# Kernel tuning notes

Measured on AMD Instinct MI355X. Metric: run time of the kernel, lower is better.

Reference implementation:

```python
import jax, jax.numpy as jnp
import numpy as np

HEADS = 16
EPS = 1e-5  # nn.LayerNorm default


def setup_inputs() -> dict:
    key = jax.random.key(0)
    ks = jax.random.split(key, 3)
    b, n, dim = 4, 1024, 1024
    x = jax.random.normal(ks[0], (b, n, dim), jnp.float32)
    ln_gamma = jnp.ones((dim,), jnp.float32)
    ln_beta = jnp.zeros((dim,), jnp.float32)
    # torch.nn.Linear stores weight as [out_features, in_features]
    w_qkv = jax.random.normal(ks[1], (3 * dim, dim), jnp.float32) * (dim ** -0.5)
    w_out = jax.random.normal(ks[2], (dim, dim), jnp.float32) * (dim ** -0.5)
    b_out = jnp.zeros((dim,), jnp.float32)
    return {"x": x, "ln_gamma": ln_gamma, "ln_beta": ln_beta,
            "w_qkv": w_qkv, "w_out": w_out, "b_out": b_out, "topk": 32}


def reference(x, ln_gamma, ln_beta, w_qkv, w_out, b_out, topk):
    b, n, dim = x.shape
    h = HEADS
    d = dim // h
    scale = d ** -0.5  # (inner_dim/heads)^-0.5 with inner_dim=dim

    # LayerNorm (biased variance, matching torch)
    mu = x.mean(-1, keepdims=True)
    var = x.var(-1, keepdims=True)
    xn = (x - mu) * jax.lax.rsqrt(var + EPS) * ln_gamma + ln_beta

    # qkv projection (no bias): y = x @ W^T
    qkv = jnp.einsum('bnd,ed->bne', xn, w_qkv)  # [b, n, 3*dim]
    q, k, v = jnp.split(qkv, 3, axis=-1)
    split_heads = lambda t: t.reshape(b, n, h, d).transpose(0, 2, 1, 3)  # [b,h,n,d]
    q = split_heads(q) * scale
    k = split_heads(k)
    v = split_heads(v)

    sim = jnp.einsum('bhid,bhjd->bhij', q, k)          # [b,h,n,n]
    attn = jax.nn.softmax(sim, axis=-1)
    # top-k SELECTION: probability values are discarded, only indices used
    _, idx = jax.lax.top_k(attn, topk)                 # [b,h,n,topk]
    # gather v rows at top-k indices and sum (unweighted), matching
    # torch.gather(vv, 2, idx).sum(-2)
    gathered = jnp.take_along_axis(
        v, idx.reshape(b, h, n * topk)[..., None], axis=2)  # [b,h,n*topk,d]
    xsum = gathered.reshape(b, h, n, topk, d).sum(axis=3)   # [b,h,n,d]

    # global min/max normalization then exp
    xmin = xsum.min()
    xmax = xsum.max()
    out = jnp.exp((xsum - xmin) / (xmax - xmin))

    out = out.transpose(0, 2, 1, 3).reshape(b, n, dim)  # b h n d -> b n (h d)
    # final projection (self.out Linear; Dropout(0.2) inert at eval)
    return jnp.einsum('bnd,ed->bne', out, w_out) + b_out
```

## Files before the change

### kernel.cpp

```cpp
#include <hip/hip_runtime.h>


#define LN_EPS 1e-5f

using half8   = __attribute__((ext_vector_type(8))) _Float16;
using half4   = __attribute__((ext_vector_type(4))) _Float16;
using float4v = __attribute__((ext_vector_type(4))) float;

__device__ __forceinline__ void gload_lds16(const void* g, void* l) {
  __builtin_amdgcn_global_load_lds(
      (const __attribute__((address_space(1))) void*)g,
      (__attribute__((address_space(3))) void*)l, 16, 0, 0);
}
__device__ __forceinline__ float4v mfma16(half8 a, half8 b, float4v c) {
  return __builtin_amdgcn_mfma_f32_16x16x32_f16(a, b, c, 0, 0, 0);
}
struct HL { _Float16 h, l; };
__device__ __forceinline__ HL split2(float x) {
  _Float16 h = (_Float16)x;
  return { h, (_Float16)(x - (float)h) };
}
__device__ __forceinline__ int mbcnt(unsigned long long m) {
  return __builtin_amdgcn_mbcnt_hi((unsigned)(m >> 32),
         __builtin_amdgcn_mbcnt_lo((unsigned)m, 0u));
}

__device__ __forceinline__ unsigned fkey(float f) {
  unsigned u = __float_as_uint(f);
  return ((int)u < 0) ? ~u : (u | 0x80000000u);
}
__device__ __forceinline__ int enc_i(float f) {
  int i = __float_as_int(f);
  return i >= 0 ? i : (i ^ 0x7fffffff);
}
__device__ __forceinline__ float dec_i(int e) {
  return __int_as_float(e >= 0 ? e : (e ^ 0x7fffffff));
}

__global__ __launch_bounds__(256)
void prep_kernel(const float* __restrict__ x, const float* __restrict__ gamma,
                 const float* __restrict__ beta,
                 _Float16* __restrict__ xh, _Float16* __restrict__ xl,
                 const float* __restrict__ wqkv, const float* __restrict__ wout,
                 _Float16* __restrict__ wqh, _Float16* __restrict__ wql,
                 _Float16* __restrict__ woh, _Float16* __restrict__ wol,
                 int* __restrict__ minmax) {
  int blk = blockIdx.x, t = threadIdx.x;
  if (blk < 4096) {
    __shared__ float red[8];
    int row = blk;
    const float4* xr = (const float4*)(x + (size_t)row * 1024);
    float4 v = xr[t];
    float s  = v.x + v.y + v.z + v.w;
    float s2 = v.x*v.x + v.y*v.y + v.z*v.z + v.w*v.w;
    #pragma unroll
    for (int o = 32; o >= 1; o >>= 1) {
      s  += __shfl_xor(s,  o, 64);
      s2 += __shfl_xor(s2, o, 64);
    }
    int w = t >> 6, l = t & 63;
    if (l == 0) { red[w*2] = s; red[w*2+1] = s2; }
    __syncthreads();
    float S  = red[0] + red[2] + red[4] + red[6];
    float S2 = red[1] + red[3] + red[5] + red[7];
    float mu  = S * (1.0f/1024.0f);
    float var = S2 * (1.0f/1024.0f) - mu*mu;
    float r = rsqrtf(var + LN_EPS);
    float4 g  = ((const float4*)gamma)[t];
    float4 bb = ((const float4*)beta)[t];
    float o0 = (v.x - mu) * r * g.x + bb.x;
    float o1 = (v.y - mu) * r * g.y + bb.y;
    float o2 = (v.z - mu) * r * g.z + bb.z;
    float o3 = (v.w - mu) * r * g.w + bb.w;
    HL r0 = split2(o0), r1 = split2(o1), r2 = split2(o2), r3 = split2(o3);
    half4 hh = { r0.h, r1.h, r2.h, r3.h };
    half4 ll = { r0.l, r1.l, r2.l, r3.l };
    size_t e = (size_t)row * 1024 + t*4;
    *(half4*)(xh + e) = hh;
    *(half4*)(xl + e) = ll;
  } else if (blk < 8192) {
    size_t i4 = (size_t)(blk - 4096) * 256 + t;
    const float* src; _Float16 *dh, *dl; size_t off;
    if (i4 < 786432) { src = wqkv; dh = wqh; dl = wql; off = i4; }
    else             { src = wout; dh = woh; dl = wol; off = i4 - 786432; }
    float4 v = ((const float4*)src)[off];
    HL r0 = split2(v.x), r1 = split2(v.y), r2 = split2(v.z), r3 = split2(v.w);
    half4 hh = { r0.h, r1.h, r2.h, r3.h };
    half4 ll = { r0.l, r1.l, r2.l, r3.l };
    ((half4*)dh)[off] = hh;
    ((half4*)dl)[off] = ll;
  } else if (t == 0) {
    minmax[0] = 0x7fffffff;
    minmax[1] = (int)0x80000000;
  }
}

template<int MODE, int NT>
__global__ __launch_bounds__(256)
void gemm_f16split(const _Float16* __restrict__ Ah, const _Float16* __restrict__ Al,
                   const _Float16* __restrict__ Bh, const _Float16* __restrict__ Bl,
                   const float* __restrict__ bias, float* __restrict__ CO,
                   _Float16* __restrict__ QH, _Float16* __restrict__ QL,
                   _Float16* __restrict__ KH, _Float16* __restrict__ KL,
                   float* __restrict__ CV) {
  constexpr int NV = NT / 32;
  __shared__ __align__(16) _Float16 lds[8192 + 2 * NT * 32];
  const int K = 1024;
  int tid = threadIdx.x, w = tid >> 6, l = tid & 63;
  int m0 = blockIdx.y * 128, n0 = blockIdx.x * NT;
  int wm = (w >> 1) * 64, wn = (w & 1) * (NT / 2);

  const _Float16* src = (w == 0) ? Ah : (w == 1) ? Al : (w == 2) ? Bh : Bl;
  int rowbase = (w < 2) ? m0 : n0;
  int iters   = (w < 2) ? 8 : NT / 16;
  _Float16* dst = lds + ((w < 2) ? (size_t)w * 4096
                                 : (size_t)8192 + (size_t)(w - 2) * NT * 32);
  int sr = l >> 2, sc = l & 3;

  float4v acc[4][NV];
  #pragma unroll
  for (int u = 0; u < 4; ++u)
    #pragma unroll
    for (int vv = 0; vv < NV; ++vv) acc[u][vv] = (float4v){0.f, 0.f, 0.f, 0.f};

  int quad = l >> 4, lo16 = l & 15;
  for (int kt = 0; kt < K; kt += 32) {
    __syncthreads();
    for (int i = 0; i < iters; ++i) {
      int row = i * 16 + sr;
      gload_lds16(src + (size_t)(rowbase + row) * K + kt + sc * 8,
                  dst + row * 32 + sc * 8);
    }
    __syncthreads();
    half8 ah[4], al[4], bh[NV], bl[NV];
    #pragma unroll
    for (int u = 0; u < 4; ++u) {
      int mrow = wm + u * 16 + lo16;
      ah[u] = *(const half8*)&lds[        (size_t)mrow * 32 + quad * 8];
      al[u] = *(const half8*)&lds[ 4096 + (size_t)mrow * 32 + quad * 8];
    }
    #pragma unroll
    for (int vv = 0; vv < NV; ++vv) {
      int nrow = wn + vv * 16 + lo16;
      bh[vv] = *(const half8*)&lds[8192           + (size_t)nrow * 32 + quad * 8];
      bl[vv] = *(const half8*)&lds[8192 + NT * 32 + (size_t)nrow * 32 + quad * 8];
    }
    #pragma unroll
    for (int u = 0; u < 4; ++u)
      #pragma unroll
      for (int vv = 0; vv < NV; ++vv) {
        acc[u][vv] = mfma16(ah[u], bh[vv], acc[u][vv]);
        acc[u][vv] = mfma16(ah[u], bl[vv], acc[u][vv]);
        acc[u][vv] = mfma16(al[u], bh[vv], acc[u][vv]);
      }
  }

  #pragma unroll
  for (int u = 0; u < 4; ++u) {
    #pragma unroll
    for (int vv = 0; vv < NV; ++vv) {
      #pragma unroll
      for (int rg = 0; rg < 4; ++rg) {
        int row = m0 + wm + u * 16 + quad * 4 + rg;
        int col = n0 + wn + vv * 16 + lo16;
        float val = acc[u][vv][rg];
        if (MODE == 0) {
          int which = col >> 10, h = (col >> 6) & 15, dd = col & 63;
          int b = row >> 10, i = row & 1023;
          size_t e = ((size_t)(b * 16 + h) << 16) + ((size_t)i << 6) + dd;
          if (which == 2) { CV[e] = val; }
          else {
            HL sp = split2(val);
            if (which == 0) { QH[e] = sp.h; QL[e] = sp.l; }
            else            { KH[e] = sp.h; KL[e] = sp.l; }
          }
        } else {
          CO[(size_t)row * 1024 + col] = val + bias[col];
        }
      }
    }
  }
}

__global__ __launch_bounds__(1024)
void attn_kernel(const _Float16* __restrict__ qh, const _Float16* __restrict__ ql,
                 const _Float16* __restrict__ kh, const _Float16* __restrict__ kl,
                 const float* __restrict__ vg, float* __restrict__ xsum) {
  __shared__ float simb[16][1028];
  __shared__ int sel[16][32];
  int g = blockIdx.x;
  int xcd = g & 7, slot = g >> 3;
  int bh = (slot >> 6) * 8 + xcd, grp = slot & 63;
  int tid = threadIdx.x, w = tid >> 6, l = tid & 63;
  int quad = l >> 4, lo16 = l & 15;
  size_t hb = (size_t)bh << 16;

  const _Float16* qhp = qh + hb + ((size_t)(grp * 16 + lo16) << 6);
  const _Float16* qlp = ql + hb + ((size_t)(grp * 16 + lo16) << 6);
  half8 ah0 = *(const half8*)(qhp + quad * 8);
  half8 ah1 = *(const half8*)(qhp + 32 + quad * 8);
  half8 al0 = *(const half8*)(qlp + quad * 8);
  half8 al1 = *(const half8*)(qlp + 32 + quad * 8);

  const _Float16* khp = kh + hb;
  const _Float16* klp = kl + hb;
  int jbase = w * 64;

  #pragma unroll
  for (int tt = 0; tt < 4; ++tt) {
    size_t off = ((size_t)(jbase + tt * 16 + lo16) << 6) + quad * 8;
    half8 b0 = *(const half8*)(khp + off);
    half8 b1 = *(const half8*)(khp + off + 32);
    half8 c0 = *(const half8*)(klp + off);
    half8 c1 = *(const half8*)(klp + off + 32);
    float4v acc = (float4v){0.f, 0.f, 0.f, 0.f};
    acc = mfma16(ah0, b0, acc);
    acc = mfma16(ah0, c0, acc);
    acc = mfma16(al0, b0, acc);
    acc = mfma16(ah1, b1, acc);
    acc = mfma16(ah1, c1, acc);
    acc = mfma16(al1, b1, acc);
    int jc = jbase + tt * 16 + lo16;
    #pragma unroll
    for (int rg = 0; rg < 4; ++rg)
      simb[quad * 4 + rg][jc] = acc[rg];
  }
  __syncthreads();

  unsigned ku[16];
  #pragma unroll
  for (int s = 0; s < 16; ++s) ku[s] = fkey(simb[w][s * 64 + l]);

  unsigned cur = 0u;
  bool exact = false;
  for (int bit = 31; bit >= 0; --bit) {
    unsigned T = cur | (1u << bit);
    int c = 0;
    #pragma unroll
    for (int s = 0; s < 16; ++s) c += __popcll(__ballot(ku[s] >= T));
    if (c >= 32) {
      cur = T;
      if (c == 32) { exact = true; break; }
    }
  }

  int base = 0;
  if (exact) {
    #pragma unroll
    for (int s = 0; s < 16; ++s) {
      bool take = ku[s] >= cur;
      unsigned long long mtk = __ballot(take);
      if (take) sel[w][base + mbcnt(mtk)] = s * 64 + l;
      base += __popcll(mtk);
    }
  } else {
    int gcnt = 0;
    #pragma unroll
    for (int s = 0; s < 16; ++s) gcnt += __popcll(__ballot(ku[s] > cur));
    int need = 32 - gcnt;
    int eqb = 0;
    #pragma unroll
    for (int s = 0; s < 16; ++s) {
      bool gt = ku[s] > cur;
      bool eq = ku[s] == cur;
      unsigned long long meq = __ballot(eq);
      int eqr = eqb + mbcnt(meq);
      bool take = gt || (eq && (eqr < need));
      unsigned long long mtk = __ballot(take);
      if (take) sel[w][base + mbcnt(mtk)] = s * 64 + l;
      base += __popcll(mtk);
      eqb  += __popcll(meq);
    }
  }

  const float* vb = vg + hb;
  int lg = l >> 4, lc = (l & 15) * 4;
  float4 vacc = {0.f, 0.f, 0.f, 0.f};
  #pragma unroll
  for (int p = 0; p < 8; ++p) {
    int j = sel[w][p * 4 + lg];
    float4 t = *(const float4*)(vb + ((size_t)j << 6) + lc);
    vacc.x += t.x; vacc.y += t.y; vacc.z += t.z; vacc.w += t.w;
  }
  #pragma unroll
  for (int o = 32; o >= 16; o >>= 1) {
    vacc.x += __shfl_xor(vacc.x, o, 64);
    vacc.y += __shfl_xor(vacc.y, o, 64);
    vacc.z += __shfl_xor(vacc.z, o, 64);
    vacc.w += __shfl_xor(vacc.w, o, 64);
  }
  if (l < 16)
    *(float4*)(xsum + hb + ((size_t)(grp * 16 + w) << 6) + l * 4) = vacc;
}

__global__ __launch_bounds__(256)
void reduce_kernel(const float* __restrict__ xsum, int* __restrict__ minmax) {
  __shared__ float red[8];
  int tid = threadIdx.x, w = tid >> 6, l = tid & 63;
  const float4* p = (const float4*)xsum + (size_t)blockIdx.x * 4096 + tid;
  float mn = 3.4e38f, mx = -3.4e38f;
  #pragma unroll
  for (int i = 0; i < 16; ++i) {
    float4 v = p[(size_t)i * 256];
    mn = fminf(mn, fminf(fminf(v.x, v.y), fminf(v.z, v.w)));
    mx = fmaxf(mx, fmaxf(fmaxf(v.x, v.y), fmaxf(v.z, v.w)));
  }
  #pragma unroll
  for (int o = 32; o >= 1; o >>= 1) {
    mn = fminf(mn, __shfl_xor(mn, o, 64));
    mx = fmaxf(mx, __shfl_xor(mx, o, 64));
  }
  if (l == 0) { red[w*2] = mn; red[w*2+1] = mx; }
  __syncthreads();
  if (tid == 0) {
    mn = fminf(fminf(red[0], red[2]), fminf(red[4], red[6]));
    mx = fmaxf(fmaxf(red[1], red[3]), fmaxf(red[5], red[7]));
    atomicMin(minmax,     enc_i(mn));
    atomicMax(minmax + 1, enc_i(mx));
  }
}

__global__ __launch_bounds__(256)
void fin_kernel(const float* __restrict__ xsum, const int* __restrict__ minmax,
                _Float16* __restrict__ oh, _Float16* __restrict__ ol) {
  int idx = blockIdx.x * 256 + threadIdx.x;
  float mn = dec_i(minmax[0]);
  float mx = dec_i(minmax[1]);
  float inv = 1.0f / (mx - mn);
  float4 xv = ((const float4*)xsum)[idx];
  float o0 = expf((xv.x - mn) * inv);
  float o1 = expf((xv.y - mn) * inv);
  float o2 = expf((xv.z - mn) * inv);
  float o3 = expf((xv.w - mn) * inv);
  HL r0 = split2(o0), r1 = split2(o1), r2 = split2(o2), r3 = split2(o3);
  half4 hh = { r0.h, r1.h, r2.h, r3.h };
  half4 ll = { r0.l, r1.l, r2.l, r3.l };
  int e0 = idx << 2;
  int bh = e0 >> 16, i = (e0 >> 6) & 1023, dd = e0 & 63;
  int b = bh >> 4, h = bh & 15;
  size_t oe = ((size_t)(b * 1024 + i) << 10) + (h << 6) + dd;
  *(half4*)(oh + oe) = hh;
  *(half4*)(ol + oe) = ll;
}

extern "C" void kernel_launch(void* const* d_in, const int* in_sizes, int n_in,
                              void* d_out, int out_size, void* d_ws, size_t ws_size,
                              hipStream_t stream) {
  const float* x     = (const float*)d_in[0];
  const float* gamma = (const float*)d_in[1];
  const float* beta  = (const float*)d_in[2];
  const float* w_qkv = (const float*)d_in[3];
  const float* w_out = (const float*)d_in[4];
  const float* b_out = (const float*)d_in[5];

  char* B = (char*)d_ws;
  const size_t MB = 1024ull * 1024ull;
  float*    v   = (float*)B;
  _Float16* qh  = (_Float16*)(B + 16*MB);
  _Float16* ql  = (_Float16*)(B + 24*MB);
  _Float16* kh  = (_Float16*)(B + 32*MB);
  _Float16* kl  = (_Float16*)(B + 40*MB);
  float*    xs  = (float*)(B + 48*MB);
  _Float16* xh  = (_Float16*)(B + 48*MB);
  _Float16* xl  = (_Float16*)(B + 56*MB);
  _Float16* woh = (_Float16*)(B + 64*MB);
  _Float16* wol = (_Float16*)(B + 66*MB);
  int*   minmax = (int*)(B + 68*MB);
  _Float16* wqh = (_Float16*)(B + 69*MB);
  _Float16* wql = (_Float16*)(B + 75*MB);
  _Float16* oth = qh;
  _Float16* otl = ql;

  prep_kernel<<<8193, 256, 0, stream>>>(x, gamma, beta, xh, xl,
                                        w_qkv, w_out, wqh, wql, woh, wol,
                                        minmax);
  gemm_f16split<0, 128><<<dim3(24, 32), 256, 0, stream>>>(
      xh, xl, wqh, wql, nullptr, nullptr, qh, ql, kh, kl, v);
  attn_kernel<<<4096, 1024, 0, stream>>>(qh, ql, kh, kl, v, xs);
  reduce_kernel<<<256, 256, 0, stream>>>(xs, minmax);
  fin_kernel<<<4096, 256, 0, stream>>>(xs, minmax, oth, otl);
  gemm_f16split<1, 64><<<dim3(16, 32), 256, 0, stream>>>(
      oth, otl, woh, wol, b_out, (float*)d_out,
      nullptr, nullptr, nullptr, nullptr, nullptr);
}
```

Measured before the change: 407.4 us.

## Fuse min/max reduction into attention and use plain fp16 for output projection

Removes the separate reduce kernel by having each attention block compute its local min/max and atomically update one of 64 per-head partial slots, which fin_kernel then reduces. The output projection drops the hi/lo fp16 split and runs a single-MFMA fp16 GEMM on a plain fp16 copy of w_out and of the exp output. This cuts one launch, the extra pass over xsum, and two-thirds of the output GEMM's MFMA work and memory traffic, at the cost of reduced precision in the final projection.

```diff
diff --git a/kernel.cpp b/kernel.cpp
--- a/kernel.cpp
+++ b/kernel.cpp
@@ -43,8 +43,8 @@
                  _Float16* __restrict__ xh, _Float16* __restrict__ xl,
                  const float* __restrict__ wqkv, const float* __restrict__ wout,
                  _Float16* __restrict__ wqh, _Float16* __restrict__ wql,
-                 _Float16* __restrict__ woh, _Float16* __restrict__ wol,
-                 int* __restrict__ minmax) {
+                 _Float16* __restrict__ woh,
+                 int* __restrict__ pmin, int* __restrict__ pmax) {
   int blk = blockIdx.x, t = threadIdx.x;
   if (blk < 4096) {
     __shared__ float red[8];
@@ -80,75 +80,72 @@
     *(half4*)(xl + e) = ll;
   } else if (blk < 8192) {
     size_t i4 = (size_t)(blk - 4096) * 256 + t;
-    const float* src; _Float16 *dh, *dl; size_t off;
-    if (i4 < 786432) { src = wqkv; dh = wqh; dl = wql; off = i4; }
-    else             { src = wout; dh = woh; dl = wol; off = i4 - 786432; }
-    float4 v = ((const float4*)src)[off];
-    HL r0 = split2(v.x), r1 = split2(v.y), r2 = split2(v.z), r3 = split2(v.w);
-    half4 hh = { r0.h, r1.h, r2.h, r3.h };
-    half4 ll = { r0.l, r1.l, r2.l, r3.l };
-    ((half4*)dh)[off] = hh;
-    ((half4*)dl)[off] = ll;
-  } else if (t == 0) {
-    minmax[0] = 0x7fffffff;
-    minmax[1] = (int)0x80000000;
-  }
-}
-
-template<int MODE, int NT>
+    if (i4 < 786432) {
+      float4 v = ((const float4*)wqkv)[i4];
+      HL r0 = split2(v.x), r1 = split2(v.y), r2 = split2(v.z), r3 = split2(v.w);
+      half4 hh = { r0.h, r1.h, r2.h, r3.h };
+      half4 ll = { r0.l, r1.l, r2.l, r3.l };
+      ((half4*)wqh)[i4] = hh;
+      ((half4*)wql)[i4] = ll;
+    } else {
+      size_t off = i4 - 786432;
+      float4 v = ((const float4*)wout)[off];
+      half4 hh = { (_Float16)v.x, (_Float16)v.y, (_Float16)v.z, (_Float16)v.w };
+      ((half4*)woh)[off] = hh;
+    }
+  } else {
+    if (t < 64)              pmin[t]      = 0x7fffffff;
+    else if (t < 128)        pmax[t - 64] = (int)0x80000000;
+  }
+}
+
 __global__ __launch_bounds__(256)
-void gemm_f16split(const _Float16* __restrict__ Ah, const _Float16* __restrict__ Al,
-                   const _Float16* __restrict__ Bh, const _Float16* __restrict__ Bl,
-                   const float* __restrict__ bias, float* __restrict__ CO,
-                   _Float16* __restrict__ QH, _Float16* __restrict__ QL,
-                   _Float16* __restrict__ KH, _Float16* __restrict__ KL,
-                   float* __restrict__ CV) {
-  constexpr int NV = NT / 32;
-  __shared__ __align__(16) _Float16 lds[8192 + 2 * NT * 32];
+void gemm_qkv(const _Float16* __restrict__ Ah, const _Float16* __restrict__ Al,
+              const _Float16* __restrict__ Bh, const _Float16* __restrict__ Bl,
+              _Float16* __restrict__ QH, _Float16* __restrict__ QL,
+              _Float16* __restrict__ KH, _Float16* __restrict__ KL,
+              float* __restrict__ CV) {
+  __shared__ __align__(16) _Float16 lds[4 * 128 * 32];
   const int K = 1024;
   int tid = threadIdx.x, w = tid >> 6, l = tid & 63;
-  int m0 = blockIdx.y * 128, n0 = blockIdx.x * NT;
-  int wm = (w >> 1) * 64, wn = (w & 1) * (NT / 2);
+  int m0 = blockIdx.y * 128, n0 = blockIdx.x * 128;
+  int wm = (w >> 1) * 64, wn = (w & 1) * 64;
 
   const _Float16* src = (w == 0) ? Ah : (w == 1) ? Al : (w == 2) ? Bh : Bl;
   int rowbase = (w < 2) ? m0 : n0;
-  int iters   = (w < 2) ? 8 : NT / 16;
-  _Float16* dst = lds + ((w < 2) ? (size_t)w * 4096
-                                 : (size_t)8192 + (size_t)(w - 2) * NT * 32);
+  _Float16* dst = lds + (size_t)w * 4096;
   int sr = l >> 2, sc = l & 3;
 
-  float4v acc[4][NV];
+  float4v acc[4][4];
   #pragma unroll
   for (int u = 0; u < 4; ++u)
     #pragma unroll
-    for (int vv = 0; vv < NV; ++vv) acc[u][vv] = (float4v){0.f, 0.f, 0.f, 0.f};
+    for (int vv = 0; vv < 4; ++vv) acc[u][vv] = (float4v){0.f, 0.f, 0.f, 0.f};
 
   int quad = l >> 4, lo16 = l & 15;
   for (int kt = 0; kt < K; kt += 32) {
     __syncthreads();
-    for (int i = 0; i < iters; ++i) {
+    #pragma unroll
+    for (int i = 0; i < 8; ++i) {
       int row = i * 16 + sr;
       gload_lds16(src + (size_t)(rowbase + row) * K + kt + sc * 8,
                   dst + row * 32 + sc * 8);
     }
     __syncthreads();
-    half8 ah[4], al[4], bh[NV], bl[NV];
+    half8 ah[4], al[4], bh[4], bl[4];
     #pragma unroll
     for (int u = 0; u < 4; ++u) {
       int mrow = wm + u * 16 + lo16;
+      int nrow = wn + u * 16 + lo16;
       ah[u] = *(const half8*)&lds[        (size_t)mrow * 32 + quad * 8];
       al[u] = *(const half8*)&lds[ 4096 + (size_t)mrow * 32 + quad * 8];
-    }
-    #pragma unroll
-    for (int vv = 0; vv < NV; ++vv) {
-      int nrow = wn + vv * 16 + lo16;
-      bh[vv] = *(const half8*)&lds[8192           + (size_t)nrow * 32 + quad * 8];
-      bl[vv] = *(const half8*)&lds[8192 + NT * 32 + (size_t)nrow * 32 + quad * 8];
+      bh[u] = *(const half8*)&lds[ 8192 + (size_t)nrow * 32 + quad * 8];
+      bl[u] = *(const half8*)&lds[12288 + (size_t)nrow * 32 + quad * 8];
     }
     #pragma unroll
     for (int u = 0; u < 4; ++u)
       #pragma unroll
-      for (int vv = 0; vv < NV; ++vv) {
+      for (int vv = 0; vv < 4; ++vv) {
         acc[u][vv] = mfma16(ah[u], bh[vv], acc[u][vv]);
         acc[u][vv] = mfma16(ah[u], bl[vv], acc[u][vv]);
         acc[u][vv] = mfma16(al[u], bh[vv], acc[u][vv]);
@@ -158,24 +155,20 @@
   #pragma unroll
   for (int u = 0; u < 4; ++u) {
     #pragma unroll
-    for (int vv = 0; vv < NV; ++vv) {
+    for (int vv = 0; vv < 4; ++vv) {
       #pragma unroll
       for (int rg = 0; rg < 4; ++rg) {
         int row = m0 + wm + u * 16 + quad * 4 + rg;
         int col = n0 + wn + vv * 16 + lo16;
         float val = acc[u][vv][rg];
-        if (MODE == 0) {
-          int which = col >> 10, h = (col >> 6) & 15, dd = col & 63;
-          int b = row >> 10, i = row & 1023;
-          size_t e = ((size_t)(b * 16 + h) << 16) + ((size_t)i << 6) + dd;
-          if (which == 2) { CV[e] = val; }
-          else {
-            HL sp = split2(val);
-            if (which == 0) { QH[e] = sp.h; QL[e] = sp.l; }
-            else            { KH[e] = sp.h; KL[e] = sp.l; }
-          }
-        } else {
-          CO[(size_t)row * 1024 + col] = val + bias[col];
+        int which = col >> 10, h = (col >> 6) & 15, dd = col & 63;
+        int b = row >> 10, i = row & 1023;
+        size_t e = ((size_t)(b * 16 + h) << 16) + ((size_t)i << 6) + dd;
+        if (which == 2) { CV[e] = val; }
+        else {
+          HL sp = split2(val);
+          if (which == 0) { QH[e] = sp.h; QL[e] = sp.l; }
+          else            { KH[e] = sp.h; KL[e] = sp.l; }
         }
       }
     }
@@ -185,9 +178,11 @@
 __global__ __launch_bounds__(1024)
 void attn_kernel(const _Float16* __restrict__ qh, const _Float16* __restrict__ ql,
                  const _Float16* __restrict__ kh, const _Float16* __restrict__ kl,
-                 const float* __restrict__ vg, float* __restrict__ xsum) {
+                 const float* __restrict__ vg, float* __restrict__ xsum,
+                 int* __restrict__ pmin, int* __restrict__ pmax) {
   __shared__ float simb[16][1028];
   __shared__ int sel[16][32];
+  __shared__ float bmn[16], bmx[16];
   int g = blockIdx.x;
   int xcd = g & 7, slot = g >> 3;
   int bh = (slot >> 6) * 8 + xcd, grp = slot & 63;
@@ -291,56 +286,116 @@
   }
   if (l < 16)
     *(float4*)(xsum + hb + ((size_t)(grp * 16 + w) << 6) + l * 4) = vacc;
+
+  float m4 = fminf(fminf(vacc.x, vacc.y), fminf(vacc.z, vacc.w));
+  float M4 = fmaxf(fmaxf(vacc.x, vacc.y), fmaxf(vacc.z, vacc.w));
+  #pragma unroll
+  for (int o = 8; o >= 1; o >>= 1) {
+    m4 = fminf(m4, __shfl_xor(m4, o, 64));
+    M4 = fmaxf(M4, __shfl_xor(M4, o, 64));
+  }
+  if (l == 0) { bmn[w] = m4; bmx[w] = M4; }
+  __syncthreads();
+  if (w == 0 && l < 16) {
+    float a = bmn[l], b2 = bmx[l];
+    #pragma unroll
+    for (int o = 8; o >= 1; o >>= 1) {
+      a  = fminf(a,  __shfl_xor(a,  o, 64));
+      b2 = fmaxf(b2, __shfl_xor(b2, o, 64));
+    }
+    if (l == 0) {
+      atomicMin(pmin + bh, enc_i(a));
+      atomicMax(pmax + bh, enc_i(b2));
+    }
+  }
 }
 
 __global__ __launch_bounds__(256)
-void reduce_kernel(const float* __restrict__ xsum, int* __restrict__ minmax) {
-  __shared__ float red[8];
-  int tid = threadIdx.x, w = tid >> 6, l = tid & 63;
-  const float4* p = (const float4*)xsum + (size_t)blockIdx.x * 4096 + tid;
-  float mn = 3.4e38f, mx = -3.4e38f;
-  #pragma unroll
-  for (int i = 0; i < 16; ++i) {
-    float4 v = p[(size_t)i * 256];
-    mn = fminf(mn, fminf(fminf(v.x, v.y), fminf(v.z, v.w)));
-    mx = fmaxf(mx, fmaxf(fmaxf(v.x, v.y), fmaxf(v.z, v.w)));
-  }
-  #pragma unroll
-  for (int o = 32; o >= 1; o >>= 1) {
-    mn = fminf(mn, __shfl_xor(mn, o, 64));
-    mx = fmaxf(mx, __shfl_xor(mx, o, 64));
-  }
-  if (l == 0) { red[w*2] = mn; red[w*2+1] = mx; }
+void fin_kernel(const float* __restrict__ xsum, const int* __restrict__ pmin,
+                const int* __restrict__ pmax, _Float16* __restrict__ oh) {
+  __shared__ float mm[2];
+  int tid = threadIdx.x;
+  if (tid < 64) {
+    float fa = dec_i(pmin[tid]);
+    float fb = dec_i(pmax[tid]);
+    #pragma unroll
+    for (int o = 32; o >= 1; o >>= 1) {
+      fa = fminf(fa, __shfl_xor(fa, o, 64));
+      fb = fmaxf(fb, __shfl_xor(fb, o, 64));
+    }
+    if (tid == 0) { mm[0] = fa; mm[1] = fb; }
+  }
   __syncthreads();
-  if (tid == 0) {
-    mn = fminf(fminf(red[0], red[2]), fminf(red[4], red[6]));
-    mx = fmaxf(fmaxf(red[1], red[3]), fmaxf(red[5], red[7]));
-    atomicMin(minmax,     enc_i(mn));
-    atomicMax(minmax + 1, enc_i(mx));
-  }
-}
-
-__global__ __launch_bounds__(256)
-void fin_kernel(const float* __restrict__ xsum, const int* __restrict__ minmax,
-                _Float16* __restrict__ oh, _Float16* __restrict__ ol) {
-  int idx = blockIdx.x * 256 + threadIdx.x;
-  float mn = dec_i(minmax[0]);
-  float mx = dec_i(minmax[1]);
-  float inv = 1.0f / (mx - mn);
+  float mn = mm[0];
+  float inv = 1.0f / (mm[1] - mn);
+  int idx = blockIdx.x * 256 + tid;
   float4 xv = ((const float4*)xsum)[idx];
-  float o0 = expf((xv.x - mn) * inv);
-  float o1 = expf((xv.y - mn) * inv);
-  float o2 = expf((xv.z - mn) * inv);
-  float o3 = expf((xv.w - mn) * inv);
-  HL r0 = split2(o0), r1 = split2(o1), r2 = split2(o2), r3 = split2(o3);
-  half4 hh = { r0.h, r1.h, r2.h, r3.h };
-  half4 ll = { r0.l, r1.l, r2.l, r3.l };
+  half4 hh = { (_Float16)expf((xv.x - mn) * inv),
+               (_Float16)expf((xv.y - mn) * inv),
+               (_Float16)expf((xv.z - mn) * inv),
+               (_Float16)expf((xv.w - mn) * inv) };
   int e0 = idx << 2;
   int bh = e0 >> 16, i = (e0 >> 6) & 1023, dd = e0 & 63;
   int b = bh >> 4, h = bh & 15;
   size_t oe = ((size_t)(b * 1024 + i) << 10) + (h << 6) + dd;
   *(half4*)(oh + oe) = hh;
-  *(half4*)(ol + oe) = ll;
+}
+
+__global__ __launch_bounds__(256)
+void gemm_out(const _Float16* __restrict__ A, const _Float16* __restrict__ Bw,
+              const float* __restrict__ bias, float* __restrict__ CO) {
+  __shared__ __align__(16) _Float16 lds[192 * 32];
+  const int K = 1024;
+  int tid = threadIdx.x, w = tid >> 6, l = tid & 63;
+  int m0 = blockIdx.y * 128, n0 = blockIdx.x * 64;
+  int wm = (w >> 1) * 64, wn = (w & 1) * 32;
+  int sr = l >> 2, sc = l & 3;
+  int quad = l >> 4, lo16 = l & 15;
+
+  float4v acc[4][2];
+  #pragma unroll
+  for (int u = 0; u < 4; ++u)
+    #pragma unroll
+    for (int vv = 0; vv < 2; ++vv) acc[u][vv] = (float4v){0.f, 0.f, 0.f, 0.f};
+
+  for (int kt = 0; kt < K; kt += 32) {
+    __syncthreads();
+    #pragma unroll
+    for (int i = 0; i < 3; ++i) {
+      int row = w * 48 + i * 16 + sr;
+      const _Float16* sp = (row < 128)
+          ? A  + (size_t)(m0 + row) * K + kt + sc * 8
+          : Bw + (size_t)(n0 + row - 128) * K + kt + sc * 8;
+      gload_lds16(sp, lds + row * 32 + sc * 8);
+    }
+    __syncthreads();
+    half8 af[4], bf[2];
+    #pragma unroll
+    for (int u = 0; u < 4; ++u)
+      af[u] = *(const half8*)&lds[(size_t)(wm + u * 16 + lo16) * 32 + quad * 8];
+    #pragma unroll
+    for (int vv = 0; vv < 2; ++vv)
+      bf[vv] = *(const half8*)&lds[(size_t)(128 + wn + vv * 16 + lo16) * 32
+                                   + quad * 8];
+    #pragma unroll
+    for (int u = 0; u < 4; ++u)
+      #pragma unroll
+      for (int vv = 0; vv < 2; ++vv)
+        acc[u][vv] = mfma16(af[u], bf[vv], acc[u][vv]);
+  }
+
+  #pragma unroll
+  for (int u = 0; u < 4; ++u) {
+    #pragma unroll
+    for (int vv = 0; vv < 2; ++vv) {
+      #pragma unroll
+      for (int rg = 0; rg < 4; ++rg) {
+        int row = m0 + wm + u * 16 + quad * 4 + rg;
+        int col = n0 + wn + vv * 16 + lo16;
+        CO[(size_t)row * 1024 + col] = acc[u][vv][rg] + bias[col];
+      }
+    }
+  }
 }
 
 extern "C" void kernel_launch(void* const* d_in, const int* in_sizes, int n_in,
@@ -364,22 +419,18 @@
   _Float16* xh  = (_Float16*)(B + 48*MB);
   _Float16* xl  = (_Float16*)(B + 56*MB);
   _Float16* woh = (_Float16*)(B + 64*MB);
-  _Float16* wol = (_Float16*)(B + 66*MB);
-  int*   minmax = (int*)(B + 68*MB);
+  int*     pmin = (int*)(B + 66*MB);
+  int*     pmax = (int*)(B + 66*MB + 4096);
   _Float16* wqh = (_Float16*)(B + 69*MB);
   _Float16* wql = (_Float16*)(B + 75*MB);
   _Float16* oth = qh;
-  _Float16* otl = ql;
 
   prep_kernel<<<8193, 256, 0, stream>>>(x, gamma, beta, xh, xl,
-                                        w_qkv, w_out, wqh, wql, woh, wol,
-                                        minmax);
-  gemm_f16split<0, 128><<<dim3(24, 32), 256, 0, stream>>>(
-      xh, xl, wqh, wql, nullptr, nullptr, qh, ql, kh, kl, v);
-  attn_kernel<<<4096, 1024, 0, stream>>>(qh, ql, kh, kl, v, xs);
-  reduce_kernel<<<256, 256, 0, stream>>>(xs, minmax);
-  fin_kernel<<<4096, 256, 0, stream>>>(xs, minmax, oth, otl);
-  gemm_f16split<1, 64><<<dim3(16, 32), 256, 0, stream>>>(
-      oth, otl, woh, wol, b_out, (float*)d_out,
-      nullptr, nullptr, nullptr, nullptr, nullptr);
-}
+                                        w_qkv, w_out, wqh, wql, woh,
+                                        pmin, pmax);
+  gemm_qkv<<<dim3(24, 32), 256, 0, stream>>>(
+      xh, xl, wqh, wql, qh, ql, kh, kl, v);
+  attn_kernel<<<4096, 1024, 0, stream>>>(qh, ql, kh, kl, v, xs, pmin, pmax);
+  fin_kernel<<<4096, 256, 0, stream>>>(xs, pmin, pmax, oth);
+  gemm_out<<<dim3(16, 32), 256, 0, stream>>>(oth, woh, b_out, (float*)d_out);
+}
```

Measured after the change: 393.7 us. 1.03x faster.
